# Performance work log

Hardware: AMD Instinct MI355X
Metric: run time of the kernel (lower is better)

Reference implementation:

```python
import jax, jax.numpy as jnp
import numpy as np

# TaskAttention config (from MultiTask_Agg defaults)
B, T, M, C, H, K = 4, 3, 4096, 768, 12, 256  # batch, num_tasks, feature tokens, dim, heads, capacity_factor
HD = C // H
SCALE = HD ** -0.5


def setup_inputs() -> dict:
    key = jax.random.key(0)
    ks = jax.random.split(key, 5)
    x = jax.random.normal(ks[0], (B, T + M, C), jnp.float32)
    # per-task q projections (torch Linear: y = x @ W.T + b)
    Wq = jax.random.normal(ks[1], (T, C, C), jnp.float32) * 0.02
    bq = jnp.zeros((T, C), jnp.float32)
    # shared kv projection
    Wkv = jax.random.normal(ks[2], (2 * C, C), jnp.float32) * 0.02
    bkv = jnp.zeros((2 * C,), jnp.float32)
    # per-task experts (bias=False)
    Wexp = jax.random.normal(ks[3], (T, C, C), jnp.float32) * 0.02
    return {"x": x, "Wq": Wq, "bq": bq, "Wkv": Wkv, "bkv": bkv, "Wexp": Wexp}


def reference(x, Wq, bq, Wkv, bkv, Wexp):
    Bs = x.shape[0]
    feat = x[:, T:, :]                                             # (B,M,C)
    fm = feat.reshape(Bs, M, H, HD).transpose(0, 2, 1, 3)          # (B,H,M,hd)
    kv = feat @ Wkv.T + bkv                                        # (B,M,2C)
    kv = kv.reshape(Bs, M, 2, H, HD).transpose(2, 0, 3, 1, 4)      # (2,B,H,M,hd)
    k, v = kv[0], kv[1]
    tasks = x[:, :T, :]                                            # (B,T,C)
    q = jnp.einsum('btc,tdc->btd', tasks, Wq) + bq                 # per-task Linear
    q = q.reshape(Bs, T, H, HD).transpose(0, 2, 1, 3)              # (B,H,T,hd)
    attn = jnp.einsum('bhtd,bhmd->bhtm', q, k) * SCALE             # (B,H,T,M)
    vals, idx = jax.lax.top_k(attn, K)                             # (B,H,T,K)
    w = jax.nn.softmax(vals, axis=-1)                              # softmax over top-k only
    # attn_token: sparse combine of v at top-k indices (scatter->matmul == gather->weighted sum, indices unique)
    v_topk = jnp.take_along_axis(v[:, :, None, :, :], idx[..., None], axis=3)   # (B,H,T,K,hd)
    attn_token = jnp.einsum('bhtk,bhtkd->bhtd', w, v_topk)
    attn_token = attn_token.transpose(0, 2, 1, 3).reshape(Bs, T, C)             # (B,T,C)
    # gather raw multihead features at top-k, weight, scatter back into dense (B,H,T,M,hd)
    f_topk = jnp.take_along_axis(fm[:, :, None, :, :], idx[..., None], axis=3) * w[..., None]
    bi = jnp.arange(Bs)[:, None, None, None]
    hi = jnp.arange(H)[None, :, None, None]
    ti = jnp.arange(T)[None, None, :, None]
    feature_pad = jnp.zeros((Bs, H, T, M, HD), x.dtype).at[bi, hi, ti, idx].set(f_topk)
    feature_pad = feature_pad.transpose(0, 2, 3, 1, 4).reshape(Bs, T, M, C)     # (B,T,M,C)
    # per-task expert linears (bias=False)
    feature_output = jnp.einsum('btmc,tdc->btmd', feature_pad, Wexp)            # (B,T,M,C)
    token_output = jnp.einsum('btc,tdc->btd', attn_token, Wexp)                 # (B,T,C)
    # task_topk_weight is all-ones => einsum 'btnc,btnc->bnc' is a sum over tasks
    feature_sum = feature_output.sum(axis=1)                                    # (B,M,C)
    return jnp.concatenate([token_output, feature_sum], axis=1)                 # (B,T+M,C)
```

## Files before the change

kernel.cpp:

```cpp
#include <hip/hip_runtime.h>
#include <hip/hip_bf16.h>

#define B_ 4
#define T_ 3
#define M_ 4096
#define C_ 768
#define H_ 12
#define K_ 256
#define HD_ 64
#define TM_ 4099
#define SCALE_ 0.125f
#define NBLK_ 144

typedef __attribute__((ext_vector_type(8))) short bf16x8;
typedef __attribute__((ext_vector_type(4))) float f32x4;

__device__ __forceinline__ unsigned keyf(float f) {
  unsigned u = __float_as_uint(f);
  return (u & 0x80000000u) ? ~u : (u | 0x80000000u);
}

__device__ __forceinline__ unsigned short f2bf(float f) {
  unsigned u = __float_as_uint(f);
  unsigned r = (u + 0x7FFFu + ((u >> 16) & 1u)) >> 16;
  return (unsigned short)r;
}
__device__ __forceinline__ float bf2f(unsigned short u) {
  return __uint_as_float(((unsigned)u) << 16);
}
__device__ __forceinline__ unsigned pk2(float a, float b) {
  return (unsigned)f2bf(a) | ((unsigned)f2bf(b) << 16);
}

__device__ __forceinline__ int block_excl_scan256(int v, int tid, int* sbuf) {
  int lane = tid & 63, wid = tid >> 6;
  int x = v;
  #pragma unroll
  for (int off = 1; off < 64; off <<= 1) {
    int y = __shfl_up(x, off, 64);
    if (lane >= off) x += y;
  }
  if (lane == 63) sbuf[wid] = x;
  __syncthreads();
  int base = 0;
  #pragma unroll
  for (int w = 0; w < 3; ++w) base += (w < wid) ? sbuf[w] : 0;
  __syncthreads();
  return base + x - v;
}


__global__ __launch_bounds__(256) void zero_bucket(uint4* __restrict__ p) {
  p[blockIdx.x * 256 + threadIdx.x] = make_uint4(0u, 0u, 0u, 0u);
}

__global__ __launch_bounds__(256) void q_kernel(const float* __restrict__ x,
                                                const float* __restrict__ Wq,
                                                const float* __restrict__ bq,
                                                float* __restrict__ qbuf) {
  int t = blockIdx.x;
  int d0 = blockIdx.y * 64;
  int tid = threadIdx.x;
  __shared__ float ar[B_][C_];
  for (int i = tid; i < B_ * C_; i += 256) {
    int bb = i / C_, c = i % C_;
    ar[bb][c] = x[((size_t)(bb * TM_ + t)) * C_ + c];
  }
  __syncthreads();
  int grp = tid >> 4, ln = tid & 15;
  #pragma unroll
  for (int j = 0; j < 4; ++j) {
    int d = d0 + grp * 4 + j;
    const float4* wr = (const float4*)(Wq + ((size_t)t * C_ + d) * C_);
    float a0 = 0.f, a1 = 0.f, a2 = 0.f, a3 = 0.f;
    #pragma unroll
    for (int it = 0; it < 12; ++it) {
      float4 w4 = wr[ln + 16 * it];
      const float4 x0 = *(const float4*)&ar[0][(ln + 16 * it) * 4];
      const float4 x1 = *(const float4*)&ar[1][(ln + 16 * it) * 4];
      const float4 x2 = *(const float4*)&ar[2][(ln + 16 * it) * 4];
      const float4 x3 = *(const float4*)&ar[3][(ln + 16 * it) * 4];
      a0 += w4.x * x0.x + w4.y * x0.y + w4.z * x0.z + w4.w * x0.w;
      a1 += w4.x * x1.x + w4.y * x1.y + w4.z * x1.z + w4.w * x1.w;
      a2 += w4.x * x2.x + w4.y * x2.y + w4.z * x2.z + w4.w * x2.w;
      a3 += w4.x * x3.x + w4.y * x3.y + w4.z * x3.z + w4.w * x3.w;
    }
    #pragma unroll
    for (int off = 1; off < 16; off <<= 1) {
      a0 += __shfl_xor(a0, off, 16);
      a1 += __shfl_xor(a1, off, 16);
      a2 += __shfl_xor(a2, off, 16);
      a3 += __shfl_xor(a3, off, 16);
    }
    if (ln == 0) {
      float bqv = bq[t * C_ + d];
      qbuf[(size_t)(0 * T_ + t) * C_ + d] = a0 + bqv;
      qbuf[(size_t)(1 * T_ + t) * C_ + d] = a1 + bqv;
      qbuf[(size_t)(2 * T_ + t) * C_ + d] = a2 + bqv;
      qbuf[(size_t)(3 * T_ + t) * C_ + d] = a3 + bqv;
    }
  }
}

__global__ __launch_bounds__(256) void sprj_kernel(const float* __restrict__ qbuf,
                                                   const float* __restrict__ Wkv,
                                                   const float* __restrict__ bkv,
                                                   float* __restrict__ sprjT,
                                                   float* __restrict__ qbb) {
  int blk = blockIdx.x;
  int j = blk % 36;
  int b = blk / 36;
  int t = j % T_;
  int h = j / T_;
  int tid = threadIdx.x;
  __shared__ float qs[HD_];
  if (tid < HD_) qs[tid] = qbuf[((size_t)(b * T_ + t)) * C_ + h * HD_ + tid];
  __syncthreads();
  if (tid == 0) {
    float s = 0.f;
    for (int i = 0; i < HD_; ++i) s += qs[i] * bkv[h * HD_ + i];
    qbb[blk] = s;
  }
  float a0 = 0.f, a1 = 0.f, a2 = 0.f;
  for (int i = 0; i < HD_; ++i) {
    const float* wr = Wkv + ((size_t)(h * HD_ + i)) * C_;
    float qi = qs[i];
    a0 += qi * wr[tid];
    a1 += qi * wr[tid + 256];
    a2 += qi * wr[tid + 512];
  }
  sprjT[((size_t)b * C_ + tid) * 36 + j] = a0;
  sprjT[((size_t)b * C_ + tid + 256) * 36 + j] = a1;
  sprjT[((size_t)b * C_ + tid + 512) * 36 + j] = a2;
}

__global__ __launch_bounds__(256) void score_kernel(const float* __restrict__ x,
                                                    const float* __restrict__ sprjT,
                                                    float* __restrict__ scp) {
  int b = blockIdx.x;
  int m0 = blockIdx.y * 256;
  int cc = blockIdx.z;
  int tid = threadIdx.x;

  __shared__ float fl[32][256];

  float acc[36];
  #pragma unroll
  for (int j = 0; j < 36; ++j) acc[j] = 0.f;

  const float* fr0 = x + ((size_t)(b * TM_ + T_ + m0 + tid)) * C_ + cc * 64;

  for (int kc = 0; kc < 2; ++kc) {
    float4 v[8];
    const float4* fr = (const float4*)(fr0 + kc * 32);
    #pragma unroll
    for (int i = 0; i < 8; ++i) v[i] = fr[i];
    __syncthreads();
    #pragma unroll
    for (int i = 0; i < 8; ++i) {
      fl[i * 4 + 0][tid] = v[i].x;
      fl[i * 4 + 1][tid] = v[i].y;
      fl[i * 4 + 2][tid] = v[i].z;
      fl[i * 4 + 3][tid] = v[i].w;
    }
    __syncthreads();
    const float* sp = sprjT + ((size_t)b * C_ + cc * 64 + kc * 32) * 36;
    #pragma unroll 4
    for (int k = 0; k < 32; ++k) {
      float f = fl[k][tid];
      const float* sr = sp + k * 36;
      #pragma unroll
      for (int j = 0; j < 36; ++j) acc[j] += f * sr[j];
    }
  }
  float* op = scp + ((size_t)cc * NBLK_ + (size_t)b * 36) * M_ + m0 + tid;
  #pragma unroll
  for (int j = 0; j < 36; ++j) op[(size_t)j * M_] = acc[j];
}

__global__ __launch_bounds__(256) void topk_kernel(const float* __restrict__ scp,
                                                   const float* __restrict__ qbb,
                                                   int* __restrict__ ibuf,
                                                   float* __restrict__ wbuf,
                                                   int* __restrict__ bucket) {
  int blk = blockIdx.x;
  int tid = threadIdx.x;

  __shared__ float sc[M_];
  __shared__ unsigned hist[256];
  __shared__ int sbuf[4];
  __shared__ int selm[K_];
  __shared__ float redf[4];
  __shared__ int sh_bin, sh_rem;

  float qb = qbb[blk];
  for (int i = tid; i < M_ / 4; i += 256) {
    float4 s = make_float4(qb, qb, qb, qb);
    #pragma unroll
    for (int cc = 0; cc < 12; ++cc) {
      float4 a = *(const float4*)&scp[((size_t)cc * NBLK_ + blk) * M_ + i * 4];
      s.x += a.x; s.y += a.y; s.z += a.z; s.w += a.w;
    }
    *(float4*)&sc[i * 4] =
        make_float4(s.x * SCALE_, s.y * SCALE_, s.z * SCALE_, s.w * SCALE_);
  }
  __syncthreads();

  unsigned prefix = 0;
  int remaining = K_;
  for (int shift = 24; shift >= 0; shift -= 8) {
    hist[tid] = 0;
    __syncthreads();
    unsigned pmask = (shift == 24) ? 0u : (0xFFFFFFFFu << (shift + 8));
    #pragma unroll 4
    for (int i = 0; i < 16; ++i) {
      unsigned k = keyf(sc[tid * 16 + i]);
      if ((k & pmask) == prefix) atomicAdd(&hist[(k >> shift) & 255u], 1u);
    }
    __syncthreads();
    int bin = 255 - tid;
    int v = (int)hist[bin];
    int cex = block_excl_scan256(v, tid, sbuf);
    if (cex < remaining && cex + v >= remaining) {
      sh_bin = bin;
      sh_rem = remaining - cex;
    }
    __syncthreads();
    prefix |= ((unsigned)sh_bin) << shift;
    remaining = sh_rem;
    __syncthreads();
  }
  const unsigned tau = prefix;
  const int r = remaining;
  const int cgt = K_ - r;

  int base = tid * 16;
  int myCnt = 0, myTie = 0;
  #pragma unroll
  for (int i = 0; i < 16; i++) {
    unsigned k = keyf(sc[base + i]);
    myCnt += (k > tau);
    myTie += (k == tau);
  }
  int offs = block_excl_scan256(myCnt, tid, sbuf);
  int toffs = block_excl_scan256(myTie, tid, sbuf);
  for (int i = 0; i < 16; i++) {
    int m = base + i;
    unsigned k = keyf(sc[m]);
    if (k > tau) {
      selm[offs++] = m;
    } else if (k == tau) {
      if (toffs < r) selm[cgt + toffs] = m;
      toffs++;
    }
  }
  __syncthreads();

  int m = selm[tid];
  float val = sc[m];
  float mx = val;
  #pragma unroll
  for (int off = 32; off > 0; off >>= 1) mx = fmaxf(mx, __shfl_xor(mx, off, 64));
  if ((tid & 63) == 0) redf[tid >> 6] = mx;
  __syncthreads();
  mx = fmaxf(fmaxf(redf[0], redf[1]), fmaxf(redf[2], redf[3]));
  float e = expf(val - mx);
  float sm = e;
  #pragma unroll
  for (int off = 32; off > 0; off >>= 1) sm += __shfl_xor(sm, off, 64);
  __syncthreads();
  if ((tid & 63) == 0) redf[tid >> 6] = sm;
  __syncthreads();
  sm = redf[0] + redf[1] + redf[2] + redf[3];
  ibuf[(size_t)blk * K_ + tid] = m;
  wbuf[(size_t)blk * K_ + tid] = e / sm;
  bucket[((size_t)(blk / 36) * M_ + m) * 36 + (blk % 36)] = tid + 1;
}

__global__ __launch_bounds__(256) void wfeat_kernel(const float* __restrict__ x,
                                                    const int* __restrict__ ibuf,
                                                    const float* __restrict__ wbuf,
                                                    float* __restrict__ wfp) {
  int blk = blockIdx.x, kc = blockIdx.y, cseg = blockIdx.z;
  int b = blk / 36;
  int tid = threadIdx.x;
  __shared__ int ml[64];
  __shared__ float wl[64];
  if (tid < 64) {
    ml[tid] = ibuf[(size_t)blk * K_ + kc * 64 + tid];
    wl[tid] = wbuf[(size_t)blk * K_ + kc * 64 + tid];
  }
  __syncthreads();
  int c = cseg * 256 + tid;
  const float* fbase = x + ((size_t)b * TM_ + T_) * C_ + c;
  float a = 0.f;
  #pragma unroll 4
  for (int kk = 0; kk < 64; ++kk) {
    a += wl[kk] * fbase[(size_t)ml[kk] * C_];
  }
  wfp[((size_t)blk * 4 + kc) * C_ + c] = a;
}

__global__ __launch_bounds__(256) void attn_token_kernel(
    const float* __restrict__ wfp, const float* __restrict__ Wkv,
    const float* __restrict__ bkv, float* __restrict__ atbuf) {
  int blk = blockIdx.x;
  int t = blk % T_;
  int h = (blk / T_) % H_;
  int b = blk / (T_ * H_);
  int tid = threadIdx.x;
  __shared__ float wfeat[C_];
  const float* p0 = wfp + ((size_t)blk * 4) * C_;
  #pragma unroll
  for (int j = 0; j < 3; ++j) {
    int c = tid + j * 256;
    wfeat[c] = p0[c] + p0[C_ + c] + p0[2 * C_ + c] + p0[3 * C_ + c];
  }
  __syncthreads();
  int grp = tid >> 4, ln = tid & 15;
  for (int rr = grp; rr < HD_; rr += 16) {
    const float4* wr = (const float4*)(Wkv + ((size_t)(C_ + h * HD_ + rr)) * C_);
    float acc = 0.f;
    #pragma unroll
    for (int it = 0; it < 12; ++it) {
      float4 wv = wr[ln + it * 16];
      const float4 fv = *(const float4*)&wfeat[(ln + it * 16) * 4];
      acc += wv.x * fv.x + wv.y * fv.y + wv.z * fv.z + wv.w * fv.w;
    }
    acc += __shfl_xor(acc, 1, 16);
    acc += __shfl_xor(acc, 2, 16);
    acc += __shfl_xor(acc, 4, 16);
    acc += __shfl_xor(acc, 8, 16);
    if (ln == 0)
      atbuf[((size_t)(b * T_ + t)) * C_ + h * HD_ + rr] =
          acc + bkv[C_ + h * HD_ + rr];
  }
}

__global__ __launch_bounds__(256) void token_out(const float* __restrict__ atbuf,
                                                 const float* __restrict__ Wexp,
                                                 float* __restrict__ out) {
  int t = blockIdx.x;
  int d0 = blockIdx.y * 64;
  int tid = threadIdx.x;
  __shared__ float ar[B_][C_];
  for (int i = tid; i < B_ * C_; i += 256) {
    int bb = i / C_, c = i % C_;
    ar[bb][c] = atbuf[((size_t)(bb * T_ + t)) * C_ + c];
  }
  __syncthreads();
  int grp = tid >> 4, ln = tid & 15;
  #pragma unroll
  for (int j = 0; j < 4; ++j) {
    int d = d0 + grp * 4 + j;
    const float4* wr = (const float4*)(Wexp + ((size_t)t * C_ + d) * C_);
    float a0 = 0.f, a1 = 0.f, a2 = 0.f, a3 = 0.f;
    #pragma unroll
    for (int it = 0; it < 12; ++it) {
      float4 w4 = wr[ln + 16 * it];
      const float4 x0 = *(const float4*)&ar[0][(ln + 16 * it) * 4];
      const float4 x1 = *(const float4*)&ar[1][(ln + 16 * it) * 4];
      const float4 x2 = *(const float4*)&ar[2][(ln + 16 * it) * 4];
      const float4 x3 = *(const float4*)&ar[3][(ln + 16 * it) * 4];
      a0 += w4.x * x0.x + w4.y * x0.y + w4.z * x0.z + w4.w * x0.w;
      a1 += w4.x * x1.x + w4.y * x1.y + w4.z * x1.z + w4.w * x1.w;
      a2 += w4.x * x2.x + w4.y * x2.y + w4.z * x2.z + w4.w * x2.w;
      a3 += w4.x * x3.x + w4.y * x3.y + w4.z * x3.z + w4.w * x3.w;
    }
    #pragma unroll
    for (int off = 1; off < 16; off <<= 1) {
      a0 += __shfl_xor(a0, off, 16);
      a1 += __shfl_xor(a1, off, 16);
      a2 += __shfl_xor(a2, off, 16);
      a3 += __shfl_xor(a3, off, 16);
    }
    if (ln == 0) {
      out[((size_t)0 * TM_ + t) * C_ + d] = a0;
      out[((size_t)1 * TM_ + t) * C_ + d] = a1;
      out[((size_t)2 * TM_ + t) * C_ + d] = a2;
      out[((size_t)3 * TM_ + t) * C_ + d] = a3;
    }
  }
}

__global__ __launch_bounds__(256) void scatter_mfma(
    const float* __restrict__ x, const float* __restrict__ Wexp,
    const int* __restrict__ ibuf, const float* __restrict__ wbuf,
    unsigned short* __restrict__ Y) {
  int th = blockIdx.x;
  int h = th / T_, t = th % T_;
  int b = blockIdx.y >> 2, ks = blockIdx.y & 3;
  int dc = blockIdx.z;
  int bht = b * 36 + th;
  int tid = threadIdx.x;

  __shared__ unsigned short fw[64][72];
  __shared__ unsigned short wt[192][72];

  {
    int kk = tid >> 2, cp = (tid & 3) * 16;
    int sel = ks * 64 + kk;
    int m = ibuf[(size_t)bht * K_ + sel];
    float w = wbuf[(size_t)bht * K_ + sel];
    const float* fr = x + ((size_t)(b * TM_) + T_ + m) * C_ + h * HD_ + cp;
    float4 f0 = *(const float4*)(fr + 0);
    float4 f1 = *(const float4*)(fr + 4);
    float4 f2 = *(const float4*)(fr + 8);
    float4 f3 = *(const float4*)(fr + 12);
    uint4 u0 = make_uint4(pk2(f0.x * w, f0.y * w), pk2(f0.z * w, f0.w * w),
                          pk2(f1.x * w, f1.y * w), pk2(f1.z * w, f1.w * w));
    uint4 u1 = make_uint4(pk2(f2.x * w, f2.y * w), pk2(f2.z * w, f2.w * w),
                          pk2(f3.x * w, f3.y * w), pk2(f3.z * w, f3.w * w));
    *(uint4*)&fw[kk][cp] = u0;
    *(uint4*)&fw[kk][cp + 8] = u1;
  }
  {
    #pragma unroll
    for (int r2 = 0; r2 < 3; ++r2) {
      int idx = r2 * 256 + tid;
      int dd = idx >> 2, cq = (idx & 3) * 16;
      const float* wr =
          Wexp + ((size_t)t * C_ + dc * 192 + dd) * C_ + h * HD_ + cq;
      float4 f0 = *(const float4*)(wr + 0);
      float4 f1 = *(const float4*)(wr + 4);
      float4 f2 = *(const float4*)(wr + 8);
      float4 f3 = *(const float4*)(wr + 12);
      uint4 u0 = make_uint4(pk2(f0.x, f0.y), pk2(f0.z, f0.w),
                            pk2(f1.x, f1.y), pk2(f1.z, f1.w));
      uint4 u1 = make_uint4(pk2(f2.x, f2.y), pk2(f2.z, f2.w),
                            pk2(f3.x, f3.y), pk2(f3.z, f3.w));
      *(uint4*)&wt[dd][cq] = u0;
      *(uint4*)&wt[dd][cq + 8] = u1;
    }
  }
  __syncthreads();

  int lane = tid & 63, wave = tid >> 6;
  int lrow = lane & 15, lk8 = (lane >> 4) * 8, g4 = (lane >> 4) * 4;

  f32x4 acc[12];
  #pragma unroll
  for (int n = 0; n < 12; ++n) acc[n] = (f32x4){0.f, 0.f, 0.f, 0.f};

  #pragma unroll
  for (int ks2 = 0; ks2 < 2; ++ks2) {
    bf16x8 a = *(const bf16x8*)&fw[wave * 16 + lrow][ks2 * 32 + lk8];
    #pragma unroll
    for (int n = 0; n < 12; ++n) {
      bf16x8 bfr = *(const bf16x8*)&wt[n * 16 + lrow][ks2 * 32 + lk8];
      acc[n] = __builtin_amdgcn_mfma_f32_16x16x32_bf16(a, bfr, acc[n], 0, 0, 0);
    }
  }

  #pragma unroll
  for (int n = 0; n < 12; ++n) {
    int d = dc * 192 + n * 16 + lrow;
    #pragma unroll
    for (int q = 0; q < 4; ++q) {
      int row = ks * 64 + wave * 16 + g4 + q;
      Y[((size_t)bht * K_ + row) * C_ + d] = f2bf(acc[n][q]);
    }
  }
}

__global__ __launch_bounds__(256) void combine_kernel(
    const unsigned short* __restrict__ Y, const int* __restrict__ bucket,
    float* __restrict__ out) {
  int wave = threadIdx.x >> 6, lane = threadIdx.x & 63;
  int bm = blockIdx.x * 4 + wave;
  int b = bm / M_, m = bm % M_;
  const int* bk = bucket + (size_t)bm * 36;
  int v = (lane < 36) ? bk[lane] : 0;
  unsigned long long mask = __ballot(v > 0);
  float a[12] = {0.f};
  while (mask) {
    int th = __ffsll((unsigned long long)mask) - 1;
    mask &= mask - 1;
    int sel = __shfl(v, th) - 1;
    const unsigned short* yr = Y + ((size_t)(b * 36 + th) * K_ + sel) * C_;
    #pragma unroll
    for (int seg = 0; seg < 3; ++seg) {
      uint2 r = *(const uint2*)(yr + seg * 256 + lane * 4);
      a[seg * 4 + 0] += bf2f((unsigned short)(r.x & 0xFFFFu));
      a[seg * 4 + 1] += bf2f((unsigned short)(r.x >> 16));
      a[seg * 4 + 2] += bf2f((unsigned short)(r.y & 0xFFFFu));
      a[seg * 4 + 3] += bf2f((unsigned short)(r.y >> 16));
    }
  }
  float* orow = out + ((size_t)b * TM_ + T_ + m) * C_;
  #pragma unroll
  for (int seg = 0; seg < 3; ++seg) {
    float4 o = make_float4(a[seg * 4 + 0], a[seg * 4 + 1], a[seg * 4 + 2],
                           a[seg * 4 + 3]);
    *(float4*)(orow + seg * 256 + lane * 4) = o;
  }
}

extern "C" void kernel_launch(void* const* d_in, const int* in_sizes, int n_in,
                              void* d_out, int out_size, void* d_ws, size_t ws_size,
                              hipStream_t stream) {
  (void)in_sizes; (void)n_in; (void)ws_size; (void)out_size;
  const float* x = (const float*)d_in[0];
  const float* Wq = (const float*)d_in[1];
  const float* bq = (const float*)d_in[2];
  const float* Wkv = (const float*)d_in[3];
  const float* bkv = (const float*)d_in[4];
  const float* Wexp = (const float*)d_in[5];
  float* out = (float*)d_out;

  char* ws = (char*)d_ws;
  float* qbuf = (float*)ws;
  float* atbuf = (float*)(ws + 36864);
  int* ibuf = (int*)(ws + 73728);
  float* wbuf = (float*)(ws + 221184);
  float* sprjT = (float*)(ws + 368640);
  float* qbb = (float*)(ws + 811008);
  float* wfp = (float*)(ws + 812032);
  int* bucket = (int*)(ws + 2581504);
  float* scp = (float*)(ws + 4940800);
  unsigned short* Ybf = (unsigned short*)(ws + 4940800);

  zero_bucket<<<576, 256, 0, stream>>>((uint4*)bucket);
  q_kernel<<<dim3(T_, 12), 256, 0, stream>>>(x, Wq, bq, qbuf);
  sprj_kernel<<<NBLK_, 256, 0, stream>>>(qbuf, Wkv, bkv, sprjT, qbb);
  score_kernel<<<dim3(B_, 16, 12), 256, 0, stream>>>(x, sprjT, scp);
  topk_kernel<<<NBLK_, 256, 0, stream>>>(scp, qbb, ibuf, wbuf, bucket);
  wfeat_kernel<<<dim3(NBLK_, 4, 3), 256, 0, stream>>>(x, ibuf, wbuf, wfp);
  attn_token_kernel<<<NBLK_, 256, 0, stream>>>(wfp, Wkv, bkv, atbuf);
  token_out<<<dim3(T_, 12), 256, 0, stream>>>(atbuf, Wexp, out);
  scatter_mfma<<<dim3(36, 16, 4), 256, 0, stream>>>(x, Wexp, ibuf, wbuf, Ybf);
  combine_kernel<<<B_ * M_ / 4, 256, 0, stream>>>(Ybf, bucket, out);
}
```

Before: 141.3 us.

## Fold bucket zeroing into sprj, split score reduction, loop scatter over d-chunks

Removes the separate zero_bucket launch by having sprj_kernel zero the bucket array. Splits the 12-way partial-score reduction out of topk_kernel into a separate, more parallel score_reduce kernel (576 blocks) that writes a global score buffer, which topk_kernel then copies into shared memory. It also makes scatter_mfma loop over the four 192-column output chunks inside each block instead of using a grid z-dimension. The weighted feature tile is then loaded once per block rather than four times, at the cost of 4x fewer blocks and serialized chunk work.

```diff
diff --git a/kernel.cpp b/kernel.cpp
--- a/kernel.cpp
+++ b/kernel.cpp
@@ -50,10 +50,6 @@
 }
 
 
-__global__ __launch_bounds__(256) void zero_bucket(uint4* __restrict__ p) {
-  p[blockIdx.x * 256 + threadIdx.x] = make_uint4(0u, 0u, 0u, 0u);
-}
-
 __global__ __launch_bounds__(256) void q_kernel(const float* __restrict__ x,
                                                 const float* __restrict__ Wq,
                                                 const float* __restrict__ bq,
@@ -106,13 +102,20 @@
                                                    const float* __restrict__ Wkv,
                                                    const float* __restrict__ bkv,
                                                    float* __restrict__ sprjT,
-                                                   float* __restrict__ qbb) {
+                                                   float* __restrict__ qbb,
+                                                   uint4* __restrict__ bucketz) {
   int blk = blockIdx.x;
   int j = blk % 36;
   int b = blk / 36;
   int t = j % T_;
   int h = j / T_;
   int tid = threadIdx.x;
+  {
+    uint4 z = make_uint4(0u, 0u, 0u, 0u);
+    int base = blk * 256 + tid;
+    #pragma unroll
+    for (int i = 0; i < 4; ++i) bucketz[i * 36864 + base] = z;
+  }
   __shared__ float qs[HD_];
   if (tid < HD_) qs[tid] = qbuf[((size_t)(b * T_ + t)) * C_ + h * HD_ + tid];
   __syncthreads();
@@ -178,8 +181,27 @@
   for (int j = 0; j < 36; ++j) op[(size_t)j * M_] = acc[j];
 }
 
-__global__ __launch_bounds__(256) void topk_kernel(const float* __restrict__ scp,
-                                                   const float* __restrict__ qbb,
+__global__ __launch_bounds__(256) void score_reduce(const float* __restrict__ scp,
+                                                    const float* __restrict__ qbb,
+                                                    float* __restrict__ scg) {
+  int blk = blockIdx.x;
+  int m = blockIdx.y * 1024 + threadIdx.x * 4;
+  float qb = qbb[blk];
+  float4 s = make_float4(qb, qb, qb, qb);
+  #pragma unroll
+  for (int cc = 0; cc < 12; ++cc) {
+    float4 a = *(const float4*)&scp[((size_t)cc * NBLK_ + blk) * M_ + m];
+    s.x += a.x; s.y += a.y; s.z += a.z; s.w += a.w;
+  }
+  float4 o;
+  o.x = s.x * SCALE_;
+  o.y = s.y * SCALE_;
+  o.z = s.z * SCALE_;
+  o.w = s.w * SCALE_;
+  *(float4*)&scg[(size_t)blk * M_ + m] = o;
+}
+
+__global__ __launch_bounds__(256) void topk_kernel(const float* __restrict__ scg,
                                                    int* __restrict__ ibuf,
                                                    float* __restrict__ wbuf,
                                                    int* __restrict__ bucket) {
@@ -193,17 +215,8 @@
   __shared__ float redf[4];
   __shared__ int sh_bin, sh_rem;
 
-  float qb = qbb[blk];
-  for (int i = tid; i < M_ / 4; i += 256) {
-    float4 s = make_float4(qb, qb, qb, qb);
-    #pragma unroll
-    for (int cc = 0; cc < 12; ++cc) {
-      float4 a = *(const float4*)&scp[((size_t)cc * NBLK_ + blk) * M_ + i * 4];
-      s.x += a.x; s.y += a.y; s.z += a.z; s.w += a.w;
-    }
-    *(float4*)&sc[i * 4] =
-        make_float4(s.x * SCALE_, s.y * SCALE_, s.z * SCALE_, s.w * SCALE_);
-  }
+  const float4* srow = (const float4*)(scg + (size_t)blk * M_);
+  for (int i = tid; i < M_ / 4; i += 256) ((float4*)sc)[i] = srow[i];
   __syncthreads();
 
   unsigned prefix = 0;
@@ -390,7 +403,6 @@
   int th = blockIdx.x;
   int h = th / T_, t = th % T_;
   int b = blockIdx.y >> 2, ks = blockIdx.y & 3;
-  int dc = blockIdx.z;
   int bht = b * 36 + th;
   int tid = threadIdx.x;
 
@@ -414,52 +426,57 @@
     *(uint4*)&fw[kk][cp] = u0;
     *(uint4*)&fw[kk][cp + 8] = u1;
   }
-  {
-    #pragma unroll
-    for (int r2 = 0; r2 < 3; ++r2) {
-      int idx = r2 * 256 + tid;
-      int dd = idx >> 2, cq = (idx & 3) * 16;
-      const float* wr =
-          Wexp + ((size_t)t * C_ + dc * 192 + dd) * C_ + h * HD_ + cq;
-      float4 f0 = *(const float4*)(wr + 0);
-      float4 f1 = *(const float4*)(wr + 4);
-      float4 f2 = *(const float4*)(wr + 8);
-      float4 f3 = *(const float4*)(wr + 12);
-      uint4 u0 = make_uint4(pk2(f0.x, f0.y), pk2(f0.z, f0.w),
-                            pk2(f1.x, f1.y), pk2(f1.z, f1.w));
-      uint4 u1 = make_uint4(pk2(f2.x, f2.y), pk2(f2.z, f2.w),
-                            pk2(f3.x, f3.y), pk2(f3.z, f3.w));
-      *(uint4*)&wt[dd][cq] = u0;
-      *(uint4*)&wt[dd][cq + 8] = u1;
-    }
-  }
   __syncthreads();
 
   int lane = tid & 63, wave = tid >> 6;
   int lrow = lane & 15, lk8 = (lane >> 4) * 8, g4 = (lane >> 4) * 4;
 
-  f32x4 acc[12];
-  #pragma unroll
-  for (int n = 0; n < 12; ++n) acc[n] = (f32x4){0.f, 0.f, 0.f, 0.f};
-
-  #pragma unroll
-  for (int ks2 = 0; ks2 < 2; ++ks2) {
-    bf16x8 a = *(const bf16x8*)&fw[wave * 16 + lrow][ks2 * 32 + lk8];
+  for (int dc = 0; dc < 4; ++dc) {
+    {
+      #pragma unroll
+      for (int r2 = 0; r2 < 3; ++r2) {
+        int idx = r2 * 256 + tid;
+        int dd = idx >> 2, cq = (idx & 3) * 16;
+        const float* wr =
+            Wexp + ((size_t)t * C_ + dc * 192 + dd) * C_ + h * HD_ + cq;
+        float4 f0 = *(const float4*)(wr + 0);
+        float4 f1 = *(const float4*)(wr + 4);
+        float4 f2 = *(const float4*)(wr + 8);
+        float4 f3 = *(const float4*)(wr + 12);
+        uint4 u0 = make_uint4(pk2(f0.x, f0.y), pk2(f0.z, f0.w),
+                              pk2(f1.x, f1.y), pk2(f1.z, f1.w));
+        uint4 u1 = make_uint4(pk2(f2.x, f2.y), pk2(f2.z, f2.w),
+                              pk2(f3.x, f3.y), pk2(f3.z, f3.w));
+        *(uint4*)&wt[dd][cq] = u0;
+        *(uint4*)&wt[dd][cq + 8] = u1;
+      }
+    }
+    __syncthreads();
+
+    f32x4 acc[12];
+    #pragma unroll
+    for (int n = 0; n < 12; ++n) acc[n] = (f32x4){0.f, 0.f, 0.f, 0.f};
+
+    #pragma unroll
+    for (int ks2 = 0; ks2 < 2; ++ks2) {
+      bf16x8 a = *(const bf16x8*)&fw[wave * 16 + lrow][ks2 * 32 + lk8];
+      #pragma unroll
+      for (int n = 0; n < 12; ++n) {
+        bf16x8 bfr = *(const bf16x8*)&wt[n * 16 + lrow][ks2 * 32 + lk8];
+        acc[n] = __builtin_amdgcn_mfma_f32_16x16x32_bf16(a, bfr, acc[n], 0, 0, 0);
+      }
+    }
+
     #pragma unroll
     for (int n = 0; n < 12; ++n) {
-      bf16x8 bfr = *(const bf16x8*)&wt[n * 16 + lrow][ks2 * 32 + lk8];
-      acc[n] = __builtin_amdgcn_mfma_f32_16x16x32_bf16(a, bfr, acc[n], 0, 0, 0);
-    }
-  }
-
-  #pragma unroll
-  for (int n = 0; n < 12; ++n) {
-    int d = dc * 192 + n * 16 + lrow;
-    #pragma unroll
-    for (int q = 0; q < 4; ++q) {
-      int row = ks * 64 + wave * 16 + g4 + q;
-      Y[((size_t)bht * K_ + row) * C_ + d] = f2bf(acc[n][q]);
-    }
+      int d = dc * 192 + n * 16 + lrow;
+      #pragma unroll
+      for (int q = 0; q < 4; ++q) {
+        int row = ks * 64 + wave * 16 + g4 + q;
+        Y[((size_t)bht * K_ + row) * C_ + d] = f2bf(acc[n][q]);
+      }
+    }
+    __syncthreads();
   }
 }
 
@@ -517,17 +534,19 @@
   float* qbb = (float*)(ws + 811008);
   float* wfp = (float*)(ws + 812032);
   int* bucket = (int*)(ws + 2581504);
-  float* scp = (float*)(ws + 4940800);
-  unsigned short* Ybf = (unsigned short*)(ws + 4940800);
-
-  zero_bucket<<<576, 256, 0, stream>>>((uint4*)bucket);
+  float* scg = (float*)(ws + 4940800);
+  float* scp = (float*)(ws + 7300096);
+  unsigned short* Ybf = (unsigned short*)(ws + 7300096);
+
   q_kernel<<<dim3(T_, 12), 256, 0, stream>>>(x, Wq, bq, qbuf);
-  sprj_kernel<<<NBLK_, 256, 0, stream>>>(qbuf, Wkv, bkv, sprjT, qbb);
+  sprj_kernel<<<NBLK_, 256, 0, stream>>>(qbuf, Wkv, bkv, sprjT, qbb,
+                                         (uint4*)bucket);
   score_kernel<<<dim3(B_, 16, 12), 256, 0, stream>>>(x, sprjT, scp);
-  topk_kernel<<<NBLK_, 256, 0, stream>>>(scp, qbb, ibuf, wbuf, bucket);
+  score_reduce<<<dim3(NBLK_, 4), 256, 0, stream>>>(scp, qbb, scg);
+  topk_kernel<<<NBLK_, 256, 0, stream>>>(scg, ibuf, wbuf, bucket);
   wfeat_kernel<<<dim3(NBLK_, 4, 3), 256, 0, stream>>>(x, ibuf, wbuf, wfp);
   attn_token_kernel<<<NBLK_, 256, 0, stream>>>(wfp, Wkv, bkv, atbuf);
   token_out<<<dim3(T_, 12), 256, 0, stream>>>(atbuf, Wexp, out);
-  scatter_mfma<<<dim3(36, 16, 4), 256, 0, stream>>>(x, Wexp, ibuf, wbuf, Ybf);
+  scatter_mfma<<<dim3(36, 16), 256, 0, stream>>>(x, Wexp, ibuf, wbuf, Ybf);
   combine_kernel<<<B_ * M_ / 4, 256, 0, stream>>>(Ybf, bucket, out);
 }
```

After: 139.0 us (median of 2 runs). About the same (-1.6%).
